# Kernel tuning notes

Measured on AMD Instinct MI355X. Metric: run time of the kernel, lower is better.

## Reference

```python
import jax, jax.numpy as jnp
import numpy as np

K = 16  # top-k, matches init kwarg k


def _topk_weighted_mean(conn, parent, k):
    """conn: [n, p] weights, parent: [p, d] -> [n, d].
    Faithful to original: argsort()[-k:] top-k, softmax over selected weights,
    then weighted sum of gathered parent rows."""
    idx = jnp.argsort(conn, axis=-1)[:, -k:]                      # [n, k]
    w = jax.nn.softmax(jnp.take_along_axis(conn, idx, axis=-1), axis=-1)  # [n, k]
    return jnp.einsum('nk,nkd->nd', w, parent[idx])               # gather + small matmul


def setup_inputs() -> dict:
    key = jax.random.key(0)
    k_ids, k_c1, k_c2, k_c3, k_root = jax.random.split(key, 5)
    objNum, clusterNums, embedDim = 200000, (1024, 256, 64), 64
    batch = 8192
    return {
        'ids': jax.random.randint(k_ids, (batch,), 0, objNum, dtype=jnp.int64)
               if jax.config.jax_enable_x64 else jax.random.randint(k_ids, (batch,), 0, objNum, dtype=jnp.int32),
        'conn1': jax.random.normal(k_c1, (objNum, clusterNums[0]), jnp.float32),
        'conn2': jax.random.normal(k_c2, (clusterNums[0], clusterNums[1]), jnp.float32),
        'conn3': jax.random.normal(k_c3, (clusterNums[1], clusterNums[2]), jnp.float32),
        'rootMatrix': jax.random.normal(k_root, (clusterNums[2], embedDim), jnp.float32),
    }


def reference(ids, conn1, conn2, conn3, rootMatrix):
    # getEmbedByLevel(2): combine rootMatrix rows -> level-2 cluster embeddings
    e2 = _topk_weighted_mean(conn3, rootMatrix, K)   # [256, d]
    # getEmbedByLevel(1): combine level-2 embeddings -> level-1 cluster embeddings
    e1 = _topk_weighted_mean(conn2, e2, K)           # [1024, d]
    # getEmbed(ids): combine level-1 embeddings per requested leaf object
    return _topk_weighted_mean(conn1[ids], e1, K)    # [B, d]
```

## Files before the change

### kernel.cpp

```cpp
#include <hip/hip_runtime.h>
#include <stdint.h>
#include <math.h>

#define WAVE 64
#define TOPK 16

__device__ __forceinline__ uint32_t f2s(float f) {
    uint32_t u = __float_as_uint(f);
    return u ^ (uint32_t)(((int32_t)u >> 31) | 0x80000000u);
}
__device__ __forceinline__ uint32_t umax32(uint32_t a, uint32_t b) { return a > b ? a : b; }
__device__ __forceinline__ uint32_t umin32(uint32_t a, uint32_t b) { return a < b ? a : b; }

template <int CTRL, int RMASK>
__device__ __forceinline__ uint32_t dppmax(uint32_t m) {
    uint32_t r = (uint32_t)__builtin_amdgcn_update_dpp((int)m, (int)m, CTRL, RMASK, 0xF, false);
    return umax32(m, r);
}
__device__ __forceinline__ uint32_t wave_umax(uint32_t m) {
    m = dppmax<0x121, 0xF>(m);
    m = dppmax<0x122, 0xF>(m);
    m = dppmax<0x124, 0xF>(m);
    m = dppmax<0x128, 0xF>(m);
    m = dppmax<0x142, 0xA>(m);
    m = dppmax<0x143, 0xC>(m);
    return (uint32_t)__builtin_amdgcn_readlane((int)m, 63);
}

template <int VPL>
__device__ __forceinline__ uint32_t gpos(int j, int lane) {
    if constexpr (VPL == 1) return (uint32_t)lane;
    else return (uint32_t)((j >> 2) * (WAVE * 4) + lane * 4 + (j & 3));
}

#define CE_(x, y) { const uint32_t h_ = umax32(x, y), l_ = umin32(x, y); (x) = h_; (y) = l_; }

template <int P>
__device__ __forceinline__ void topk_select(const float* __restrict__ crow,
                                            const int lane,
                                            uint32_t* __restrict__ idx) {
    constexpr int VPL = P / WAVE;
    constexpr uint32_t IMASK = (uint32_t)(P - 1);

    uint32_t k[VPL];
    if constexpr (VPL == 1) {
        k[0] = (f2s(crow[lane]) & ~IMASK) | (uint32_t)lane;
    } else {
#pragma unroll
        for (int c = 0; c < VPL / 4; ++c) {
            float4 f4 = *reinterpret_cast<const float4*>(crow + c * (WAVE * 4) + lane * 4);
            const uint32_t b = (uint32_t)(c * (WAVE * 4) + lane * 4);
            k[c * 4 + 0] = (f2s(f4.x) & ~IMASK) | (b + 0u);
            k[c * 4 + 1] = (f2s(f4.y) & ~IMASK) | (b + 1u);
            k[c * 4 + 2] = (f2s(f4.z) & ~IMASK) | (b + 2u);
            k[c * 4 + 3] = (f2s(f4.w) & ~IMASK) | (b + 3u);
        }
#pragma unroll
        for (int size = 2; size <= VPL; size <<= 1) {
#pragma unroll
            for (int stride = size >> 1; stride > 0; stride >>= 1) {
#pragma unroll
                for (int i = 0; i < VPL; ++i) {
                    const int j = i ^ stride;
                    if (j > i) {
                        if ((i & size) == 0) { CE_(k[i], k[j]); }
                        else                 { CE_(k[j], k[i]); }
                    }
                }
            }
        }
    }

    uint32_t q16 = 0;
#pragma unroll
    for (int t = 0; t < TOPK; ++t) {
        const uint32_t K = wave_umax(k[0]);
        idx[t] = K & IMASK;
        if (t == TOPK - 1) q16 = K & ~IMASK;
        const bool won = (k[0] == K);
#pragma unroll
        for (int j = 0; j < VPL - 1; ++j) k[j] = won ? k[j + 1] : k[j];
        k[VPL - 1] = won ? 0u : k[VPL - 1];
    }
    const uint32_t k17 = wave_umax(k[0]);

    if ((k17 & ~IMASK) == q16) {
        uint32_t v[VPL];
        if constexpr (VPL == 1) {
            v[0] = f2s(crow[lane]);
        } else {
#pragma unroll
            for (int c = 0; c < VPL / 4; ++c) {
                float4 f4 = *reinterpret_cast<const float4*>(crow + c * (WAVE * 4) + lane * 4);
                v[c * 4 + 0] = f2s(f4.x);
                v[c * 4 + 1] = f2s(f4.y);
                v[c * 4 + 2] = f2s(f4.z);
                v[c * 4 + 3] = f2s(f4.w);
            }
        }
#pragma unroll
        for (int t = 0; t < TOPK; ++t) {
            uint32_t m = v[0];
            int li = 0;
#pragma unroll
            for (int j = 1; j < VPL; ++j) {
                bool c = v[j] >= m;
                m = c ? v[j] : m;
                li = c ? j : li;
            }
            uint32_t gi = gpos<VPL>(li, lane);
            const uint32_t mygi = gi;
            uint32_t mm = m;
#pragma unroll
            for (int off = 32; off > 0; off >>= 1) {
                uint32_t om = (uint32_t)__shfl_xor((int)mm, off);
                uint32_t og = (uint32_t)__shfl_xor((int)gi, off);
                bool c = (om > mm) || (om == mm && og > gi);
                mm = c ? om : mm;
                gi = c ? og : gi;
            }
            idx[t] = gi;
            const bool won = (mygi == gi) && (m == mm);
#pragma unroll
            for (int j = 0; j < VPL; ++j) {
                if (won && j == li) v[j] = 0u;
            }
        }
    }
}

__device__ __forceinline__ void topk_select_1024(const float* __restrict__ crow,
                                                 const int lane,
                                                 uint32_t* __restrict__ idx) {
    constexpr uint32_t IMASK = 1023u;

    uint32_t k[16];
#pragma unroll
    for (int c = 0; c < 4; ++c) {
        float4 f4 = *reinterpret_cast<const float4*>(crow + c * (WAVE * 4) + lane * 4);
        const uint32_t b = (uint32_t)(c * (WAVE * 4) + lane * 4);
        k[c * 4 + 0] = (f2s(f4.x) & ~IMASK) | (b + 0u);
        k[c * 4 + 1] = (f2s(f4.y) & ~IMASK) | (b + 1u);
        k[c * 4 + 2] = (f2s(f4.z) & ~IMASK) | (b + 2u);
        k[c * 4 + 3] = (f2s(f4.w) & ~IMASK) | (b + 3u);
    }
#pragma unroll
    for (int c = 0; c < 4; ++c) {
        CE_(k[4 * c + 0], k[4 * c + 1]); CE_(k[4 * c + 2], k[4 * c + 3]);
        CE_(k[4 * c + 0], k[4 * c + 2]); CE_(k[4 * c + 1], k[4 * c + 3]);
        CE_(k[4 * c + 1], k[4 * c + 2]);
    }
    uint32_t h[4], g[4], t[4], r[12];
#pragma unroll
    for (int i = 0; i < 4; ++i) { h[i] = umax32(k[i], k[7 - i]); r[i] = umin32(k[i], k[7 - i]); }
    CE_(h[0], h[2]); CE_(h[1], h[3]); CE_(h[0], h[1]); CE_(h[2], h[3]);
#pragma unroll
    for (int i = 0; i < 4; ++i) { g[i] = umax32(k[8 + i], k[15 - i]); r[4 + i] = umin32(k[8 + i], k[15 - i]); }
    CE_(g[0], g[2]); CE_(g[1], g[3]); CE_(g[0], g[1]); CE_(g[2], g[3]);
#pragma unroll
    for (int i = 0; i < 4; ++i) { t[i] = umax32(h[i], g[3 - i]); r[8 + i] = umin32(h[i], g[3 - i]); }
    CE_(t[0], t[2]); CE_(t[1], t[3]); CE_(t[0], t[1]); CE_(t[2], t[3]);

    uint32_t q16 = 0;
#pragma unroll
    for (int tt = 0; tt < TOPK; ++tt) {
        if (__any(t[0] == 0u)) {
            const bool need = (t[0] == 0u);
            uint32_t rm = r[0];
#pragma unroll
            for (int j = 1; j < 12; ++j) rm = umax32(rm, r[j]);
#pragma unroll
            for (int j = 0; j < 12; ++j) r[j] = (need && r[j] == rm) ? 0u : r[j];
            t[0] = need ? rm : t[0];
        }
        const uint32_t K = wave_umax(t[0]);
        idx[tt] = K & IMASK;
        if (tt == TOPK - 1) q16 = K & ~IMASK;
        const bool won = (t[0] == K);
        t[0] = won ? t[1] : t[0];
        t[1] = won ? t[2] : t[1];
        t[2] = won ? t[3] : t[2];
        t[3] = won ? 0u : t[3];
    }
    if (__any(t[0] == 0u)) {
        const bool need = (t[0] == 0u);
        uint32_t rm = r[0];
#pragma unroll
        for (int j = 1; j < 12; ++j) rm = umax32(rm, r[j]);
        t[0] = need ? rm : t[0];
    }
    const uint32_t k17 = wave_umax(t[0]);

    if ((k17 & ~IMASK) == q16) {
        uint32_t v[16];
#pragma unroll
        for (int c = 0; c < 4; ++c) {
            float4 f4 = *reinterpret_cast<const float4*>(crow + c * (WAVE * 4) + lane * 4);
            v[c * 4 + 0] = f2s(f4.x);
            v[c * 4 + 1] = f2s(f4.y);
            v[c * 4 + 2] = f2s(f4.z);
            v[c * 4 + 3] = f2s(f4.w);
        }
#pragma unroll
        for (int tt = 0; tt < TOPK; ++tt) {
            uint32_t m = v[0];
            int li = 0;
#pragma unroll
            for (int j = 1; j < 16; ++j) {
                bool c = v[j] >= m;
                m = c ? v[j] : m;
                li = c ? j : li;
            }
            uint32_t gi = gpos<16>(li, lane);
            const uint32_t mygi = gi;
            uint32_t mm = m;
#pragma unroll
            for (int off = 32; off > 0; off >>= 1) {
                uint32_t om = (uint32_t)__shfl_xor((int)mm, off);
                uint32_t og = (uint32_t)__shfl_xor((int)gi, off);
                bool c = (om > mm) || (om == mm && og > gi);
                mm = c ? om : mm;
                gi = c ? og : gi;
            }
            idx[tt] = gi;
            const bool won = (mygi == gi) && (m == mm);
#pragma unroll
            for (int j = 0; j < 16; ++j) {
                if (won && j == li) v[j] = 0u;
            }
        }
    }
}

template <int P>
__global__ void topk_wm_kernel(const float* __restrict__ conn,
                               const float* __restrict__ parent,
                               float* __restrict__ out,
                               int n) {
    const int lane = threadIdx.x & (WAVE - 1);
    const int row = blockIdx.x * (blockDim.x >> 6) + (threadIdx.x >> 6);
    if (row >= n) return;

    const float* __restrict__ crow = conn + (long)row * P;

    uint32_t idx[TOPK];
    topk_select<P>(crow, lane, idx);

    float vsel[TOPK];
#pragma unroll
    for (int t = 0; t < TOPK; ++t) vsel[t] = crow[idx[t]];
    const float v0 = vsel[0];
    float ssum = 0.f, acc = 0.f;
#pragma unroll
    for (int t = 0; t < TOPK; ++t) {
        const float w = __expf(vsel[t] - v0);
        ssum += w;
        acc = fmaf(w, parent[idx[t] * 64u + (uint32_t)lane], acc);
    }
    out[(long)row * 64 + lane] = acc / ssum;
}

#define K3_BLOCKS 1024

__global__ void leaf_kernel(const int* __restrict__ ids,
                            const float* __restrict__ conn1,
                            const float* __restrict__ e1,
                            float* __restrict__ out,
                            int batch) {
    const int lane = threadIdx.x & (WAVE - 1);
    const int wid = blockIdx.x * (blockDim.x >> 6) + (threadIdx.x >> 6);
    const int nw = K3_BLOCKS * 4;

    for (int row = wid; row < batch; row += nw) {
        const float* __restrict__ crow = conn1 + (long)ids[row] * 1024;

        uint32_t idx[TOPK];
        topk_select_1024(crow, lane, idx);

        float vsel[TOPK];
#pragma unroll
        for (int t = 0; t < TOPK; ++t) vsel[t] = crow[idx[t]];
        const float v0 = vsel[0];
        float ssum = 0.f, acc = 0.f;
#pragma unroll
        for (int t = 0; t < TOPK; ++t) {
            const float w = __expf(vsel[t] - v0);
            ssum += w;
            acc = fmaf(w, e1[idx[t] * 64u + (uint32_t)lane], acc);
        }
        out[(long)row * 64 + lane] = acc / ssum;
    }
}

extern "C" void kernel_launch(void* const* d_in, const int* in_sizes, int n_in,
                              void* d_out, int out_size, void* d_ws, size_t ws_size,
                              hipStream_t stream) {
    const int* ids = (const int*)d_in[0];
    const float* conn1 = (const float*)d_in[1];
    const float* conn2 = (const float*)d_in[2];
    const float* conn3 = (const float*)d_in[3];
    const float* root = (const float*)d_in[4];
    float* out = (float*)d_out;

    const int batch = in_sizes[0];
    const int n1 = 1024, n2 = 256;

    float* e2 = (float*)d_ws;
    float* e1 = e2 + (size_t)n2 * 64;

    topk_wm_kernel<64><<<dim3(n2 / 4), dim3(256), 0, stream>>>(conn3, root, e2, n2);

    topk_wm_kernel<256><<<dim3(n1 / 4), dim3(256), 0, stream>>>(conn2, e2, e1, n1);

    leaf_kernel<<<dim3(K3_BLOCKS), dim3(256), 0, stream>>>(ids, conn1, e1, out, batch);
}
```

Measured before the change: 33.16 us.

## Fuse level-2 and level-1 top-k kernels with flag-based inter-block sync

Merges the two small top-k weighted-mean launches into one kernel. The first 64 blocks compute the level-2 embeddings and set per-row ready flags with release stores. All blocks then do their level-1 top-k selection and spin on the flags before gathering from e2. This removes one kernel launch and its boundary, and lets the conn2 top-k overlap with the e2 computation. In exchange it adds a memset launch, spin-waiting with a bounded timeout, and atomic loads, and it relies on all producer blocks being co-resident.

Result: slower. 45.21 us (+36.4%).

```diff
diff --git a/kernel.cpp b/kernel.cpp
--- a/kernel.cpp
+++ b/kernel.cpp
@@ -4,6 +4,19 @@
 
 #define WAVE 64
 #define TOPK 16
+
+__device__ __forceinline__ uint32_t aload_u32(const uint32_t* p) {
+    return __hip_atomic_load(p, __ATOMIC_RELAXED, __HIP_MEMORY_SCOPE_AGENT);
+}
+__device__ __forceinline__ float aload_f32(const float* p) {
+    return __hip_atomic_load(p, __ATOMIC_RELAXED, __HIP_MEMORY_SCOPE_AGENT);
+}
+__device__ __forceinline__ void astore_f32(float* p, float v) {
+    __hip_atomic_store(p, v, __ATOMIC_RELAXED, __HIP_MEMORY_SCOPE_AGENT);
+}
+__device__ __forceinline__ void astore_rel_u32(uint32_t* p, uint32_t v) {
+    __hip_atomic_store(p, v, __ATOMIC_RELEASE, __HIP_MEMORY_SCOPE_AGENT);
+}
 
 __device__ __forceinline__ uint32_t f2s(float f) {
     uint32_t u = __float_as_uint(f);
@@ -232,32 +245,66 @@
     }
 }
 
-template <int P>
-__global__ void topk_wm_kernel(const float* __restrict__ conn,
-                               const float* __restrict__ parent,
-                               float* __restrict__ out,
-                               int n) {
+__global__ void __launch_bounds__(256)
+fused12_kernel(const float* __restrict__ conn2,
+               const float* __restrict__ conn3,
+               const float* __restrict__ root,
+               uint32_t* __restrict__ fe2,
+               float* __restrict__ e2,
+               float* __restrict__ e1,
+               int n1) {
     const int lane = threadIdx.x & (WAVE - 1);
-    const int row = blockIdx.x * (blockDim.x >> 6) + (threadIdx.x >> 6);
-    if (row >= n) return;
-
-    const float* __restrict__ crow = conn + (long)row * P;
-
+    const int wib = threadIdx.x >> 6;
+    const int row = blockIdx.x * 4 + wib;
+
+    if (blockIdx.x < 64) {
+        const int prow = row;
+        const float* __restrict__ c3 = conn3 + prow * 64;
+        uint32_t pidx[TOPK];
+        topk_select<64>(c3, lane, pidx);
+        float pv[TOPK];
+#pragma unroll
+        for (int t = 0; t < TOPK; ++t) pv[t] = c3[pidx[t]];
+        const float pv0 = pv[0];
+        float ps = 0.f, pa = 0.f;
+#pragma unroll
+        for (int t = 0; t < TOPK; ++t) {
+            const float w = __expf(pv[t] - pv0);
+            ps += w;
+            pa = fmaf(w, root[pidx[t] * 64u + (uint32_t)lane], pa);
+        }
+        astore_f32(&e2[prow * 64 + lane], pa / ps);
+        asm volatile("s_waitcnt vmcnt(0)" ::: "memory");
+        if (lane == 0) astore_rel_u32(&fe2[prow], 1u);
+    }
+
+    const float* __restrict__ crow = conn2 + (long)row * 256;
     uint32_t idx[TOPK];
-    topk_select<P>(crow, lane, idx);
-
+    topk_select<256>(crow, lane, idx);
     float vsel[TOPK];
 #pragma unroll
     for (int t = 0; t < TOPK; ++t) vsel[t] = crow[idx[t]];
+
+    {
+        int spins = 0;
+        for (;;) {
+            uint32_t ok = aload_u32(fe2 + lane) & aload_u32(fe2 + lane + 64) &
+                          aload_u32(fe2 + lane + 128) & aload_u32(fe2 + lane + 192);
+            if (__all(ok == 1u)) break;
+            __builtin_amdgcn_s_sleep(8);
+            if (++spins > (1 << 20)) break;
+        }
+    }
+
     const float v0 = vsel[0];
     float ssum = 0.f, acc = 0.f;
 #pragma unroll
     for (int t = 0; t < TOPK; ++t) {
         const float w = __expf(vsel[t] - v0);
         ssum += w;
-        acc = fmaf(w, parent[idx[t] * 64u + (uint32_t)lane], acc);
-    }
-    out[(long)row * 64 + lane] = acc / ssum;
+        acc = fmaf(w, aload_f32(&e2[idx[t] * 64u + (uint32_t)lane]), acc);
+    }
+    e1[(long)row * 64 + lane] = acc / ssum;
 }
 
 #define K3_BLOCKS 1024
@@ -303,14 +350,15 @@
     float* out = (float*)d_out;
 
     const int batch = in_sizes[0];
-    const int n1 = 1024, n2 = 256;
-
-    float* e2 = (float*)d_ws;
-    float* e1 = e2 + (size_t)n2 * 64;
-
-    topk_wm_kernel<64><<<dim3(n2 / 4), dim3(256), 0, stream>>>(conn3, root, e2, n2);
-
-    topk_wm_kernel<256><<<dim3(n1 / 4), dim3(256), 0, stream>>>(conn2, e2, e1, n1);
+    const int n1 = 1024;
+
+    uint32_t* fe2 = (uint32_t*)d_ws;
+    float* e2 = (float*)((char*)d_ws + 1024);
+    float* e1 = e2 + (size_t)256 * 64;
+
+    hipMemsetAsync(fe2, 0, 256 * sizeof(uint32_t), stream);
+
+    fused12_kernel<<<dim3(256), dim3(256), 0, stream>>>(conn2, conn3, root, fe2, e2, e1, n1);
 
     leaf_kernel<<<dim3(K3_BLOCKS), dim3(256), 0, stream>>>(ids, conn1, e1, out, batch);
 }
```

## Overlap leaf top-k selection with cluster embedding build, split gather into second kernel

Applied to the files above, without the earlier changes.

Replaces the three-kernel chain with two kernels. The first runs the level-1 cluster embedding build, recomputing each level-2 embedding inline instead of storing it, in some blocks, while the remaining blocks do the independent leaf top-k selection and write weights, indices and softmax sums to workspace. A second kernel then gathers e1 rows using the stored weights and indices. This removes one launch and the serial dependency between the leaf top-k and the upper levels. In exchange it recomputes each level-2 embedding 16 times per level-1 row and adds a workspace round trip.

New measurement: 45.16 us. 36.2% more time.

```diff
diff --git a/kernel.cpp b/kernel.cpp
--- a/kernel.cpp
+++ b/kernel.cpp
@@ -232,63 +232,135 @@
     }
 }
 
-template <int P>
-__global__ void topk_wm_kernel(const float* __restrict__ conn,
-                               const float* __restrict__ parent,
-                               float* __restrict__ out,
-                               int n) {
-    const int lane = threadIdx.x & (WAVE - 1);
-    const int row = blockIdx.x * (blockDim.x >> 6) + (threadIdx.x >> 6);
-    if (row >= n) return;
-
-    const float* __restrict__ crow = conn + (long)row * P;
-
+__device__ __attribute__((noinline)) float e2val(const float* __restrict__ c3,
+                                                 const float* __restrict__ root,
+                                                 const int lane) {
     uint32_t idx[TOPK];
-    topk_select<P>(crow, lane, idx);
-
+    topk_select<64>(c3, lane, idx);
     float vsel[TOPK];
 #pragma unroll
-    for (int t = 0; t < TOPK; ++t) vsel[t] = crow[idx[t]];
+    for (int t = 0; t < TOPK; ++t) vsel[t] = c3[idx[t]];
     const float v0 = vsel[0];
     float ssum = 0.f, acc = 0.f;
 #pragma unroll
     for (int t = 0; t < TOPK; ++t) {
         const float w = __expf(vsel[t] - v0);
         ssum += w;
-        acc = fmaf(w, parent[idx[t] * 64u + (uint32_t)lane], acc);
-    }
-    out[(long)row * 64 + lane] = acc / ssum;
-}
-
-#define K3_BLOCKS 1024
-
-__global__ void leaf_kernel(const int* __restrict__ ids,
-                            const float* __restrict__ conn1,
-                            const float* __restrict__ e1,
-                            float* __restrict__ out,
-                            int batch) {
+        acc = fmaf(w, root[idx[t] * 64u + (uint32_t)lane], acc);
+    }
+    return acc / ssum;
+}
+
+#define K2_BLOCKS 256
+#define LEAF_BLOCKS 768
+
+__global__ void __launch_bounds__(256, 2)
+nodeA_kernel(const int* __restrict__ ids,
+             const float* __restrict__ conn1,
+             const float* __restrict__ conn2,
+             const float* __restrict__ conn3,
+             const float* __restrict__ root,
+             float* __restrict__ e1,
+             float* __restrict__ wbuf,
+             uint32_t* __restrict__ ibuf,
+             float* __restrict__ sbuf,
+             int batch) {
+    const int lane = threadIdx.x & (WAVE - 1);
+    const int wib = threadIdx.x >> 6;
+    const int bid = blockIdx.x;
+
+    if (bid < K2_BLOCKS) {
+        const int row = bid * 4 + wib;
+        const float* __restrict__ crow = conn2 + (long)row * 256;
+        uint32_t idx[TOPK];
+        topk_select<256>(crow, lane, idx);
+        float vsel[TOPK];
+#pragma unroll
+        for (int t = 0; t < TOPK; ++t) vsel[t] = crow[idx[t]];
+        const float v0 = vsel[0];
+        float w[TOPK];
+        float ssum = 0.f;
+#pragma unroll
+        for (int t = 0; t < TOPK; ++t) {
+            w[t] = __expf(vsel[t] - v0);
+            ssum += w[t];
+        }
+        float acc = 0.f;
+#pragma unroll
+        for (int t = 0; t < TOPK; ++t) {
+            acc = fmaf(w[t], e2val(conn3 + idx[t] * 64u, root, lane), acc);
+        }
+        e1[(long)row * 64 + lane] = acc / ssum;
+    } else {
+        const int wid = (bid - K2_BLOCKS) * 4 + wib;
+        for (int row = wid; row < batch; row += LEAF_BLOCKS * 4) {
+            const float* __restrict__ crow = conn1 + (long)ids[row] * 1024;
+            uint32_t idx[TOPK];
+            topk_select_1024(crow, lane, idx);
+            float vsel[TOPK];
+#pragma unroll
+            for (int t = 0; t < TOPK; ++t) vsel[t] = crow[idx[t]];
+            const float v0 = vsel[0];
+            float w[TOPK];
+            float ssum = 0.f;
+#pragma unroll
+            for (int t = 0; t < TOPK; ++t) {
+                w[t] = __expf(vsel[t] - v0);
+                ssum += w[t];
+            }
+            float myw = w[0];
+            uint32_t myi = idx[0];
+#pragma unroll
+            for (int t = 1; t < TOPK; ++t) {
+                myw = (lane == t) ? w[t] : myw;
+                myi = (lane == t) ? idx[t] : myi;
+            }
+            if (lane < TOPK) {
+                wbuf[(long)row * 16 + lane] = myw;
+                ibuf[(long)row * 16 + lane] = myi;
+            }
+            if (lane == 0) sbuf[row] = ssum;
+        }
+    }
+}
+
+#define B_BLOCKS 1024
+
+__global__ void __launch_bounds__(256, 4)
+nodeB_kernel(const float* __restrict__ e1,
+             const float* __restrict__ wbuf,
+             const uint32_t* __restrict__ ibuf,
+             const float* __restrict__ sbuf,
+             float* __restrict__ out,
+             int batch) {
     const int lane = threadIdx.x & (WAVE - 1);
     const int wid = blockIdx.x * (blockDim.x >> 6) + (threadIdx.x >> 6);
-    const int nw = K3_BLOCKS * 4;
-
-    for (int row = wid; row < batch; row += nw) {
-        const float* __restrict__ crow = conn1 + (long)ids[row] * 1024;
-
-        uint32_t idx[TOPK];
-        topk_select_1024(crow, lane, idx);
-
-        float vsel[TOPK];
-#pragma unroll
-        for (int t = 0; t < TOPK; ++t) vsel[t] = crow[idx[t]];
-        const float v0 = vsel[0];
-        float ssum = 0.f, acc = 0.f;
-#pragma unroll
-        for (int t = 0; t < TOPK; ++t) {
-            const float w = __expf(vsel[t] - v0);
-            ssum += w;
-            acc = fmaf(w, e1[idx[t] * 64u + (uint32_t)lane], acc);
-        }
-        out[(long)row * 64 + lane] = acc / ssum;
+
+    for (int row = wid; row < batch; row += B_BLOCKS * 4) {
+        const float4* wp = reinterpret_cast<const float4*>(wbuf + (long)row * 16);
+        const float4 w0 = wp[0], w1 = wp[1], w2 = wp[2], w3 = wp[3];
+        const uint4* ip = reinterpret_cast<const uint4*>(ibuf + (long)row * 16);
+        const uint4 i0 = ip[0], i1 = ip[1], i2 = ip[2], i3 = ip[3];
+
+        float acc = 0.f;
+        acc = fmaf(w0.x, e1[i0.x * 64u + (uint32_t)lane], acc);
+        acc = fmaf(w0.y, e1[i0.y * 64u + (uint32_t)lane], acc);
+        acc = fmaf(w0.z, e1[i0.z * 64u + (uint32_t)lane], acc);
+        acc = fmaf(w0.w, e1[i0.w * 64u + (uint32_t)lane], acc);
+        acc = fmaf(w1.x, e1[i1.x * 64u + (uint32_t)lane], acc);
+        acc = fmaf(w1.y, e1[i1.y * 64u + (uint32_t)lane], acc);
+        acc = fmaf(w1.z, e1[i1.z * 64u + (uint32_t)lane], acc);
+        acc = fmaf(w1.w, e1[i1.w * 64u + (uint32_t)lane], acc);
+        acc = fmaf(w2.x, e1[i2.x * 64u + (uint32_t)lane], acc);
+        acc = fmaf(w2.y, e1[i2.y * 64u + (uint32_t)lane], acc);
+        acc = fmaf(w2.z, e1[i2.z * 64u + (uint32_t)lane], acc);
+        acc = fmaf(w2.w, e1[i2.w * 64u + (uint32_t)lane], acc);
+        acc = fmaf(w3.x, e1[i3.x * 64u + (uint32_t)lane], acc);
+        acc = fmaf(w3.y, e1[i3.y * 64u + (uint32_t)lane], acc);
+        acc = fmaf(w3.z, e1[i3.z * 64u + (uint32_t)lane], acc);
+        acc = fmaf(w3.w, e1[i3.w * 64u + (uint32_t)lane], acc);
+
+        out[(long)row * 64 + lane] = acc / sbuf[row];
     }
 }
 
@@ -303,14 +375,15 @@
     float* out = (float*)d_out;
 
     const int batch = in_sizes[0];
-    const int n1 = 1024, n2 = 256;
-
-    float* e2 = (float*)d_ws;
-    float* e1 = e2 + (size_t)n2 * 64;
-
-    topk_wm_kernel<64><<<dim3(n2 / 4), dim3(256), 0, stream>>>(conn3, root, e2, n2);
-
-    topk_wm_kernel<256><<<dim3(n1 / 4), dim3(256), 0, stream>>>(conn2, e2, e1, n1);
-
-    leaf_kernel<<<dim3(K3_BLOCKS), dim3(256), 0, stream>>>(ids, conn1, e1, out, batch);
-}
+
+    float* e1 = (float*)d_ws;
+    float* wbuf = e1 + 1024 * 64;
+    uint32_t* ibuf = (uint32_t*)(wbuf + 8192 * 16);
+    float* sbuf = (float*)(ibuf + 8192 * 16);
+
+    nodeA_kernel<<<dim3(K2_BLOCKS + LEAF_BLOCKS), dim3(256), 0, stream>>>(
+        ids, conn1, conn2, conn3, root, e1, wbuf, ibuf, sbuf, batch);
+
+    nodeB_kernel<<<dim3(B_BLOCKS), dim3(256), 0, stream>>>(
+        e1, wbuf, ibuf, sbuf, out, batch);
+}
```

## Fuse level-2 and level-1 stages into one kernel with LDS-resident e2

Applied to the files above, without the earlier changes.

Merges the two small top-k stages into a single kernel. Each of the 64 blocks recomputes all 256 level-2 embeddings into shared memory, then computes 16 level-1 rows from LDS. This removes one kernel launch and the global round-trip for e2, at the cost of redundant level-2 computation in every block. The leaf kernel also switches from a grid-stride loop over 1024 blocks to one wave per row with batch/4 blocks.

New measurement: 84.75 us. +155.6%, slower.

```diff
diff --git a/kernel.cpp b/kernel.cpp
--- a/kernel.cpp
+++ b/kernel.cpp
@@ -232,20 +232,40 @@
     }
 }
 
-template <int P>
-__global__ void topk_wm_kernel(const float* __restrict__ conn,
-                               const float* __restrict__ parent,
-                               float* __restrict__ out,
-                               int n) {
+#define F12_BLOCKS 64
+
+__global__ void __launch_bounds__(1024)
+fused12_lds(const float* __restrict__ conn2,
+            const float* __restrict__ conn3,
+            const float* __restrict__ root,
+            float* __restrict__ e1) {
+    __shared__ float e2s[256 * 64];
     const int lane = threadIdx.x & (WAVE - 1);
-    const int row = blockIdx.x * (blockDim.x >> 6) + (threadIdx.x >> 6);
-    if (row >= n) return;
-
-    const float* __restrict__ crow = conn + (long)row * P;
-
+    const int wib = threadIdx.x >> 6;
+
+    for (int r = wib; r < 256; r += 16) {
+        const float* __restrict__ c3 = conn3 + r * 64;
+        uint32_t idx[TOPK];
+        topk_select<64>(c3, lane, idx);
+        float vsel[TOPK];
+#pragma unroll
+        for (int t = 0; t < TOPK; ++t) vsel[t] = c3[idx[t]];
+        const float v0 = vsel[0];
+        float ssum = 0.f, acc = 0.f;
+#pragma unroll
+        for (int t = 0; t < TOPK; ++t) {
+            const float w = __expf(vsel[t] - v0);
+            ssum += w;
+            acc = fmaf(w, root[idx[t] * 64u + (uint32_t)lane], acc);
+        }
+        e2s[r * 64 + lane] = acc / ssum;
+    }
+    __syncthreads();
+
+    const int row = blockIdx.x * 16 + wib;
+    const float* __restrict__ crow = conn2 + (long)row * 256;
     uint32_t idx[TOPK];
-    topk_select<P>(crow, lane, idx);
-
+    topk_select<256>(crow, lane, idx);
     float vsel[TOPK];
 #pragma unroll
     for (int t = 0; t < TOPK; ++t) vsel[t] = crow[idx[t]];
@@ -255,12 +275,10 @@
     for (int t = 0; t < TOPK; ++t) {
         const float w = __expf(vsel[t] - v0);
         ssum += w;
-        acc = fmaf(w, parent[idx[t] * 64u + (uint32_t)lane], acc);
-    }
-    out[(long)row * 64 + lane] = acc / ssum;
-}
-
-#define K3_BLOCKS 1024
+        acc = fmaf(w, e2s[idx[t] * 64u + (uint32_t)lane], acc);
+    }
+    e1[(long)row * 64 + lane] = acc / ssum;
+}
 
 __global__ void leaf_kernel(const int* __restrict__ ids,
                             const float* __restrict__ conn1,
@@ -268,28 +286,26 @@
                             float* __restrict__ out,
                             int batch) {
     const int lane = threadIdx.x & (WAVE - 1);
-    const int wid = blockIdx.x * (blockDim.x >> 6) + (threadIdx.x >> 6);
-    const int nw = K3_BLOCKS * 4;
-
-    for (int row = wid; row < batch; row += nw) {
-        const float* __restrict__ crow = conn1 + (long)ids[row] * 1024;
-
-        uint32_t idx[TOPK];
-        topk_select_1024(crow, lane, idx);
-
-        float vsel[TOPK];
-#pragma unroll
-        for (int t = 0; t < TOPK; ++t) vsel[t] = crow[idx[t]];
-        const float v0 = vsel[0];
-        float ssum = 0.f, acc = 0.f;
-#pragma unroll
-        for (int t = 0; t < TOPK; ++t) {
-            const float w = __expf(vsel[t] - v0);
-            ssum += w;
-            acc = fmaf(w, e1[idx[t] * 64u + (uint32_t)lane], acc);
-        }
-        out[(long)row * 64 + lane] = acc / ssum;
-    }
+    const int row = blockIdx.x * (blockDim.x >> 6) + (threadIdx.x >> 6);
+    if (row >= batch) return;
+
+    const float* __restrict__ crow = conn1 + (long)ids[row] * 1024;
+
+    uint32_t idx[TOPK];
+    topk_select_1024(crow, lane, idx);
+
+    float vsel[TOPK];
+#pragma unroll
+    for (int t = 0; t < TOPK; ++t) vsel[t] = crow[idx[t]];
+    const float v0 = vsel[0];
+    float ssum = 0.f, acc = 0.f;
+#pragma unroll
+    for (int t = 0; t < TOPK; ++t) {
+        const float w = __expf(vsel[t] - v0);
+        ssum += w;
+        acc = fmaf(w, e1[idx[t] * 64u + (uint32_t)lane], acc);
+    }
+    out[(long)row * 64 + lane] = acc / ssum;
 }
 
 extern "C" void kernel_launch(void* const* d_in, const int* in_sizes, int n_in,
@@ -303,14 +319,10 @@
     float* out = (float*)d_out;
 
     const int batch = in_sizes[0];
-    const int n1 = 1024, n2 = 256;
-
-    float* e2 = (float*)d_ws;
-    float* e1 = e2 + (size_t)n2 * 64;
-
-    topk_wm_kernel<64><<<dim3(n2 / 4), dim3(256), 0, stream>>>(conn3, root, e2, n2);
-
-    topk_wm_kernel<256><<<dim3(n1 / 4), dim3(256), 0, stream>>>(conn2, e2, e1, n1);
-
-    leaf_kernel<<<dim3(K3_BLOCKS), dim3(256), 0, stream>>>(ids, conn1, e1, out, batch);
-}
+
+    float* e1 = (float*)d_ws;
+
+    fused12_lds<<<dim3(F12_BLOCKS), dim3(1024), 0, stream>>>(conn2, conn3, root, e1);
+
+    leaf_kernel<<<dim3(batch / 4), dim3(256), 0, stream>>>(ids, conn1, e1, out, batch);
+}
```
